# Performance work log

Hardware: AMD Instinct MI355X
Metric: run time of the kernel (lower is better)

## Reference

```python
import jax, jax.numpy as jnp
import numpy as np

# Static configuration (matches init_kwargs)
NW, WH, WW, SH, SW = 1024, 8, 8, 2, 2
EMBED, NH = 192, 6
HD = EMBED // NH            # 32
NP = WH * WW                # 64 patches per window
S2 = SH * SW                # 4 shuffle groups
L = NP * S2                 # 256 tokens per window
NWM = 64                    # number of mask windows
SCALE = HD ** (-0.5) / SH   # head_dim**-0.5 / shuffle
EPS = 1e-5


def _rel_pos_index():
    # Swin-style relative position index for an (8,8) window.
    coords = np.stack(np.meshgrid(np.arange(WH), np.arange(WW), indexing='ij')).reshape(2, -1)
    rel = (coords[:, :, None] - coords[:, None, :]).transpose(1, 2, 0)  # (64,64,2)
    rel[..., 0] += WH - 1
    rel[..., 0] *= 2 * WW - 1
    rel[..., 1] += WW - 1
    return jnp.asarray(rel.sum(-1).reshape(-1))  # (4096,) values in [0, 225)

REL_IDX = _rel_pos_index()


def _group(x):
    # 'nw (wh sh ww sw) ch -> nw (wh ww) (sh sw) ch'
    return x.reshape(NW, WH, SH, WW, SW, EMBED).transpose(0, 1, 3, 2, 4, 5).reshape(NW, NP, S2, EMBED)


def _ungroup(x):
    # 'nw (wh ww) (sh sw) ch -> nw (wh sh ww sw) ch'
    return x.reshape(NW, WH, WW, SH, SW, EMBED).transpose(0, 1, 3, 2, 4, 5).reshape(NW, L, EMBED)


def _ln(x, w, b):
    # LayerNorm over the last two dims [shuffle**2, embed_dim]
    mu = x.mean(axis=(-2, -1), keepdims=True)
    var = x.var(axis=(-2, -1), keepdims=True)
    return (x - mu) * jax.lax.rsqrt(var + EPS) * w + b


def _heads(x):
    # 'nw np s2 (nh hd) -> nw nh np s2 hd'
    return x.reshape(NW, NP, S2, NH, HD).transpose(0, 3, 1, 2, 4)


def setup_inputs() -> dict:
    key = jax.random.key(0)
    ks = jax.random.split(key, 7)
    inp = {
        'query': jax.random.normal(ks[0], (NW, L, EMBED), jnp.float32),
        'key': jax.random.normal(ks[1], (NW, L, EMBED), jnp.float32),
        'value': jax.random.normal(ks[2], (NW, L, EMBED), jnp.float32),
        'mask': jax.random.normal(ks[3], (NWM, NP, NP), jnp.float32),
        'ln_q_w': jnp.ones((S2, EMBED), jnp.float32),
        'ln_q_b': jnp.zeros((S2, EMBED), jnp.float32),
        'ln_k_w': jnp.ones((S2, EMBED), jnp.float32),
        'ln_k_b': jnp.zeros((S2, EMBED), jnp.float32),
        'ln_v_w': jnp.ones((S2, EMBED), jnp.float32),
        'ln_v_b': jnp.zeros((S2, EMBED), jnp.float32),
        'bias_table': 0.02 * jax.random.normal(ks[4], ((2 * WH - 1) * (2 * WW - 1), NH), jnp.float32),
        'proj_w': 0.02 * jax.random.normal(ks[5], (EMBED, EMBED), jnp.float32),  # nn.Linear weight (out,in)
    }
    return inp


def reference(query, key, value, mask, ln_q_w, ln_q_b, ln_k_w, ln_k_b, ln_v_w, ln_v_b, bias_table, proj_w):
    q = _heads(_ln(_group(query), ln_q_w, ln_q_b)) * SCALE   # (nw,nh,np,s2,hd)
    k = _heads(_ln(_group(key), ln_k_w, ln_k_b))
    v = _heads(_ln(_group(value), ln_v_w, ln_v_b))

    attn = jnp.einsum('whqsc,whksc->whqk', q, k)              # (nw,nh,np,np)

    bias = bias_table[REL_IDX].reshape(NP, NP, NH).transpose(2, 0, 1)  # (nh,np,np)
    attn = attn + bias[None]

    b = NW // NWM
    attn = (attn.reshape(b, NWM, NH, NP, NP) + mask[None, :, None]).reshape(NW, NH, NP, NP)

    attn = jax.nn.softmax(attn, axis=-1)

    out = jnp.einsum('whqk,whksc->whqsc', attn, v)            # (nw,nh,np,s2,hd)
    out = out.transpose(0, 2, 3, 1, 4).reshape(NW, NP, S2, EMBED)
    out = _ungroup(out)                                       # (nw, L, embed)
    return out @ proj_w.T
```

## Files before the change

### kernel.cpp

```cpp
#include <hip/hip_runtime.h>

#define NWIN 1024
#define LTOK 256
#define EMB  192
#define NPAT 64
#define NHEAD 6
#define HDIM 32
#define SCALE 0.08838834764831845f
#define LN_EPS 1e-5f

typedef float f32x4 __attribute__((ext_vector_type(4)));
typedef short s16x8 __attribute__((ext_vector_type(8)));

#define OFF_KH  0
#define OFF_VT  16384
#define OFF_PB  32768
#define OFF_OB  40960
#define OFF_ST  57856
#define OFF_BH  59392
#define OFF_HB  60416
#define SMEM_BYTES 61440
#define OBSTRIDE 264

__device__ __forceinline__ unsigned short f2bf(float f) {
    unsigned u = __float_as_uint(f);
    u += 0x7fffu + ((u >> 16) & 1u);
    return (unsigned short)(u >> 16);
}

__device__ __forceinline__ int tok_of(int p, int s) {
    return ((p >> 3) << 5) + ((s >> 1) << 4) + ((p & 7) << 1) + (s & 1);
}

__device__ __forceinline__ f32x4 mfma16(s16x8 a, s16x8 b, f32x4 c) {
    return __builtin_amdgcn_mfma_f32_16x16x32_bf16(a, b, c, 0, 0, 0);
}

__device__ __forceinline__ s16x8 ln_pack8r(const float* v, float mu, float rs,
                                           const float* __restrict__ wl,
                                           const float* __restrict__ bl,
                                           float scale) {
    f32x4 w0 = *(const f32x4*)wl;
    f32x4 w1 = *(const f32x4*)(wl + 4);
    f32x4 c0 = *(const f32x4*)bl;
    f32x4 c1 = *(const f32x4*)(bl + 4);
    s16x8 r;
    r[0] = (short)f2bf(((v[0]-mu)*rs*w0[0] + c0[0])*scale);
    r[1] = (short)f2bf(((v[1]-mu)*rs*w0[1] + c0[1])*scale);
    r[2] = (short)f2bf(((v[2]-mu)*rs*w0[2] + c0[2])*scale);
    r[3] = (short)f2bf(((v[3]-mu)*rs*w0[3] + c0[3])*scale);
    r[4] = (short)f2bf(((v[4]-mu)*rs*w1[0] + c1[0])*scale);
    r[5] = (short)f2bf(((v[5]-mu)*rs*w1[1] + c1[1])*scale);
    r[6] = (short)f2bf(((v[6]-mu)*rs*w1[2] + c1[2])*scale);
    r[7] = (short)f2bf(((v[7]-mu)*rs*w1[3] + c1[3])*scale);
    return r;
}

__device__ __forceinline__ void ln_f8r(const float* v, float mu, float rs,
                                       const float* __restrict__ wl,
                                       const float* __restrict__ bl,
                                       float* o) {
    f32x4 w0 = *(const f32x4*)wl;
    f32x4 w1 = *(const f32x4*)(wl + 4);
    f32x4 c0 = *(const f32x4*)bl;
    f32x4 c1 = *(const f32x4*)(bl + 4);
    o[0] = (v[0]-mu)*rs*w0[0] + c0[0];
    o[1] = (v[1]-mu)*rs*w0[1] + c0[1];
    o[2] = (v[2]-mu)*rs*w0[2] + c0[2];
    o[3] = (v[3]-mu)*rs*w0[3] + c0[3];
    o[4] = (v[4]-mu)*rs*w1[0] + c1[0];
    o[5] = (v[5]-mu)*rs*w1[1] + c1[1];
    o[6] = (v[6]-mu)*rs*w1[2] + c1[2];
    o[7] = (v[7]-mu)*rs*w1[3] + c1[3];
}

__device__ __forceinline__ void load_T8(const float* __restrict__ g, size_t wbase,
                                        int tid, int hh, float pre[2][8]) {
    int p = tid & 63;
    #pragma unroll
    for (int i = 0; i < 2; ++i) {
        int scb = (tid >> 6) * 2 + i;
        int s = scb >> 2, cbx = scb & 3;
        int t = tok_of(p, s);
        const float* gp = g + wbase + t*EMB + hh*HDIM + cbx*8;
        *(f32x4*)&pre[i][0] = *(const f32x4*)gp;
        *(f32x4*)&pre[i][4] = *(const f32x4*)(gp + 4);
    }
}

__device__ __forceinline__ void stage_K(char* smem, int tid, int hh,
                                        const float kpre[2][8], const float* stats,
                                        const float* __restrict__ lnkw,
                                        const float* __restrict__ lnkb) {
    const float* muk = stats + 128; const float* rsk = stats + 192;
    int p = tid & 63;
    #pragma unroll
    for (int i = 0; i < 2; ++i) {
        int scb = (tid >> 6) * 2 + i;
        int s = scb >> 2, cbx = scb & 3;
        int chb = hh*HDIM + cbx*8;
        s16x8 kk = ln_pack8r(kpre[i], muk[p], rsk[p],
                             lnkw + s*EMB + chb, lnkb + s*EMB + chb, 1.0f);
        *(s16x8*)(smem + OFF_KH + p*256 + ((scb*16) ^ ((p & 7) << 4))) = kk;
    }
}

__device__ __forceinline__ void stage_V(char* smem, int tid, int hh,
                                        const float vpre[2][8], const float* stats,
                                        const float* __restrict__ lnvw,
                                        const float* __restrict__ lnvb) {
    const float* muv = stats + 256; const float* rsv = stats + 320;
    int p = tid & 63;
    #pragma unroll
    for (int i = 0; i < 2; ++i) {
        int scb = (tid >> 6) * 2 + i;
        int s = scb >> 2, cbx = scb & 3;
        int chb = hh*HDIM + cbx*8;
        float vn[8];
        ln_f8r(vpre[i], muv[p], rsv[p], lnvw + s*EMB + chb, lnvb + s*EMB + chb, vn);
        #pragma unroll
        for (int j = 0; j < 8; ++j) {
            int sc = scb*8 + j;
            *(unsigned short*)(smem + OFF_VT + sc*128 + ((p*2) ^ ((sc & 7) << 4)))
                = f2bf(vn[j]);
        }
    }
}


__global__ __launch_bounds__(512, 2) void dwa_attn_kernel(
    const float* __restrict__ q_g, const float* __restrict__ k_g,
    const float* __restrict__ v_g, const float* __restrict__ mask_g,
    const float* __restrict__ lnqw, const float* __restrict__ lnqb,
    const float* __restrict__ lnkw, const float* __restrict__ lnkb,
    const float* __restrict__ lnvw, const float* __restrict__ lnvb,
    const float* __restrict__ btab, float* __restrict__ out_g)
{
    __shared__ __align__(16) char smem[SMEM_BYTES];

    const int tid  = threadIdx.x;
    const int lane = tid & 63;
    const int wv   = tid >> 6;
    const int win  = blockIdx.x;
    const size_t wbase = (size_t)win * LTOK * EMB;
    char* preb = (char*)out_g + (size_t)win * 196608 + 98304;

    float* stats = (float*)(smem + OFF_ST);
    float* muq = stats;       float* rsq = stats + 64;
    float* biash = (float*)(smem + OFF_BH);
    float2* HB = (float2*)(smem + OFF_HB);

    const int mstrip = wv >> 1, nhalf = wv & 1;
    const int l15 = lane & 15, l4 = lane >> 4;
    const int pr = mstrip*16 + l15;
    const int cb = l4;

    const float* mask_w = mask_g + (size_t)(win & 63) * NPAT * NPAT;
    const int kc0 = nhalf*32 + l15, kc1 = kc0 + 16;
    float mm0[4], mm1[4];
    int idx0[4], idx1[4];
    {
        int kh0 = kc0 >> 3, kw0 = kc0 & 7, kh1 = kc1 >> 3, kw1 = kc1 & 7;
        #pragma unroll
        for (int r = 0; r < 4; ++r) {
            int qr = mstrip*16 + l4*4 + r;
            mm0[r] = mask_w[qr*64 + kc0];
            mm1[r] = mask_w[qr*64 + kc1];
            idx0[r] = ((qr>>3) - kh0 + 7)*15 + ((qr&7) - kw0 + 7);
            idx1[r] = ((qr>>3) - kh1 + 7)*15 + ((qr&7) - kw1 + 7);
        }
    }

    {
        float* part = (float*)(smem + OFF_OB);
        const int t = tid >> 1, half = tid & 1;
        const f32x4* qp = (const f32x4*)(q_g + wbase + t*EMB + half*96);
        const f32x4* kp = (const f32x4*)(k_g + wbase + t*EMB + half*96);
        const f32x4* vp = (const f32x4*)(v_g + wbase + t*EMB + half*96);
        float s1q=0.f,s2q=0.f,s1k=0.f,s2k=0.f,s1v=0.f,s2v=0.f;
        #pragma unroll 4
        for (int i = 0; i < 24; ++i) {
            f32x4 a = qp[i];
            s1q += a[0]+a[1]+a[2]+a[3];
            s2q += a[0]*a[0]+a[1]*a[1]+a[2]*a[2]+a[3]*a[3];
            f32x4 b = kp[i];
            s1k += b[0]+b[1]+b[2]+b[3];
            s2k += b[0]*b[0]+b[1]*b[1]+b[2]*b[2]+b[3]*b[3];
            f32x4 c = vp[i];
            s1v += c[0]+c[1]+c[2]+c[3];
            s2v += c[0]*c[0]+c[1]*c[1]+c[2]*c[2]+c[3]*c[3];
        }
        float* pp = part + (t*2 + half)*6;
        pp[0]=s1q; pp[1]=s2q; pp[2]=s1k; pp[3]=s2k; pp[4]=s1v; pp[5]=s2v;
        __syncthreads();
        if (tid < NPAT) {
            float S[6] = {0.f,0.f,0.f,0.f,0.f,0.f};
            #pragma unroll
            for (int s = 0; s < 4; ++s) {
                int tt = tok_of(tid, s);
                const float* pr_ = part + tt*12;
                #pragma unroll
                for (int x = 0; x < 6; ++x) S[x] += pr_[x] + pr_[6 + x];
            }
            #pragma unroll
            for (int x = 0; x < 3; ++x) {
                float mu  = S[2*x] * (1.f/768.f);
                float var = S[2*x+1] * (1.f/768.f) - mu*mu;
                stats[x*128 + tid]      = mu;
                stats[x*128 + 64 + tid] = rsqrtf(var + LN_EPS);
            }
        }
        __syncthreads();
    }

    float kpre[2][8], vpre[2][8];
    float breg;
    load_T8(k_g, wbase, tid, 0, kpre);
    load_T8(v_g, wbase, tid, 0, vpre);
    breg = (tid < 225) ? btab[tid * NHEAD] : 0.f;
    stage_K(smem, tid, 0, kpre, stats, lnkw, lnkb);
    stage_V(smem, tid, 0, vpre, stats, lnvw, lnvb);
    if (tid < 225) biash[tid] = breg;
    __syncthreads();

    for (int h = 0; h < NHEAD; ++h) {
        const bool pf = (h < NHEAD-1);
        if (pf) {
            load_T8(k_g, wbase, tid, h+1, kpre);
            load_T8(v_g, wbase, tid, h+1, vpre);
            breg = (tid < 225) ? btab[tid*NHEAD + h + 1] : 0.f;
        }

        float e0[4], e1[4], mrow[4];
        {
            float mu = muq[pr], rs = rsq[pr];
            const float* qbase = q_g + wbase + h*HDIM + cb*8;
            f32x4 acc0 = {0.f,0.f,0.f,0.f};
            f32x4 acc1 = {0.f,0.f,0.f,0.f};
            #pragma unroll
            for (int ks = 0; ks < 4; ++ks) {
                int t = tok_of(pr, ks);
                float qv[8];
                *(f32x4*)&qv[0] = *(const f32x4*)(qbase + t*EMB);
                *(f32x4*)&qv[4] = *(const f32x4*)(qbase + t*EMB + 4);
                int chb = h*HDIM + cb*8;
                s16x8 af = ln_pack8r(qv, mu, rs,
                                     lnqw + ks*EMB + chb, lnqb + ks*EMB + chb, SCALE);
                {
                    int row = nhalf*32 + l15;
                    s16x8 bf = *(const s16x8*)(smem + OFF_KH + row*256 +
                                  ((ks*64 + cb*16) ^ ((row & 7) << 4)));
                    acc0 = mfma16(af, bf, acc0);
                }
                {
                    int row = nhalf*32 + 16 + l15;
                    s16x8 bf = *(const s16x8*)(smem + OFF_KH + row*256 +
                                  ((ks*64 + cb*16) ^ ((row & 7) << 4)));
                    acc1 = mfma16(af, bf, acc1);
                }
            }
            float srow[4];
            #pragma unroll
            for (int r = 0; r < 4; ++r) {
                float L0 = acc0[r] + mm0[r] + biash[idx0[r]];
                float L1 = acc1[r] + mm1[r] + biash[idx1[r]];
                float m = fmaxf(L0, L1);
                m = fmaxf(m, __shfl_xor(m, 1));
                m = fmaxf(m, __shfl_xor(m, 2));
                m = fmaxf(m, __shfl_xor(m, 4));
                m = fmaxf(m, __shfl_xor(m, 8));
                float a = __expf(L0 - m), b = __expf(L1 - m);
                float s = a + b;
                s += __shfl_xor(s, 1);
                s += __shfl_xor(s, 2);
                s += __shfl_xor(s, 4);
                s += __shfl_xor(s, 8);
                e0[r] = a; e1[r] = b; mrow[r] = m; srow[r] = s;
            }
            if (l15 == 0) {
                #pragma unroll
                for (int r = 0; r < 4; ++r) {
                    float2 v; v.x = mrow[r]; v.y = srow[r];
                    HB[(mstrip*16 + l4*4 + r)*2 + nhalf] = v;
                }
            }
        }
        __syncthreads();

        if (pf) {
            stage_K(smem, tid, h+1, kpre, stats, lnkw, lnkb);
            if (tid < 225) biash[tid] = breg;
        }
        #pragma unroll
        for (int r = 0; r < 4; ++r) {
            int qr = mstrip*16 + l4*4 + r;
            float2 ha = HB[qr*2 + 0], hb = HB[qr*2 + 1];
            float M = fmaxf(ha.x, hb.x);
            float tot = ha.y*__expf(ha.x - M) + hb.y*__expf(hb.x - M);
            float f = __expf(mrow[r] - M) / tot;
            unsigned short p0 = f2bf(e0[r]*f);
            unsigned short p1 = f2bf(e1[r]*f);
            *(unsigned short*)(smem + OFF_PB + qr*128 + ((kc0*2) ^ ((qr & 7) << 4))) = p0;
            *(unsigned short*)(smem + OFF_PB + qr*128 + ((kc1*2) ^ ((qr & 7) << 4))) = p1;
        }
        __syncthreads();

        {
            s16x8 ap0 = *(const s16x8*)(smem + OFF_PB + pr*128 +
                          ((cb*16) ^ ((pr & 7) << 4)));
            s16x8 ap1 = *(const s16x8*)(smem + OFF_PB + pr*128 +
                          ((64 + cb*16) ^ ((pr & 7) << 4)));
            __builtin_amdgcn_s_setprio(1);
            #pragma unroll
            for (int i = 0; i < 4; ++i) {
                int nt = nhalf*4 + i;
                int brow = nt*16 + l15;
                f32x4 acc = {0.f,0.f,0.f,0.f};
                s16x8 bf0 = *(const s16x8*)(smem + OFF_VT + brow*128 +
                              ((cb*16) ^ ((brow & 7) << 4)));
                s16x8 bf1 = *(const s16x8*)(smem + OFF_VT + brow*128 +
                              ((64 + cb*16) ^ ((brow & 7) << 4)));
                acc = mfma16(ap0, bf0, acc);
                acc = mfma16(ap1, bf1, acc);
                int sc = nt*16 + l15;
                #pragma unroll
                for (int r = 0; r < 4; ++r) {
                    int qp = mstrip*16 + l4*4 + r;
                    *(unsigned short*)(smem + OFF_OB + qp*OBSTRIDE + sc*2) = f2bf(acc[r]);
                }
            }
            __builtin_amdgcn_s_setprio(0);
        }
        __syncthreads();

        #pragma unroll
        for (int i = 0; i < 2; ++i) {
            int c = i*512 + tid;
            int qp = c >> 4, ch = c & 15;
            s16x8 v = *(const s16x8*)(smem + OFF_OB + qp*OBSTRIDE + ch*16);
            *(s16x8*)(preb + h*16384 + qp*256 + ch*16) = v;
        }
        if (pf) stage_V(smem, tid, h+1, vpre, stats, lnvw, lnvb);
    }
}

__global__ __launch_bounds__(256, 2) void dwa_proj_kernel(
    const float* __restrict__ pw, float* __restrict__ out_g)
{
    __shared__ __align__(16) char smem[73728];

    const int tid  = threadIdx.x;
    const int lane = tid & 63;
    const int wv   = tid >> 6;
    const int w    = blockIdx.x;
    const char* preb = (const char*)out_g + (size_t)w * 196608 + 98304;
    const int cb = lane >> 4;

    s16x8 af[4][6];
    #pragma unroll
    for (int si = 0; si < 4; ++si) {
        int t = (wv*4 + si)*16 + (lane & 15);
        int qp = ((t >> 5) << 3) | ((t >> 1) & 7);
        int s  = (((t >> 4) & 1) << 1) | (t & 1);
        #pragma unroll
        for (int ks = 0; ks < 6; ++ks)
            af[si][ks] = *(const s16x8*)(preb + ks*16384 + qp*256 + s*64 + cb*16);
    }

    #pragma unroll 2
    for (int i = 0; i < 18; ++i) {
        int c = i*256 + tid;
        int orow = c / 24, cb8 = c % 24;
        const float* wp = pw + (size_t)orow*EMB + cb8*8;
        f32x4 a = *(const f32x4*)wp;
        f32x4 b = *(const f32x4*)(wp + 4);
        s16x8 w8;
        w8[0] = (short)f2bf(a[0]); w8[1] = (short)f2bf(a[1]);
        w8[2] = (short)f2bf(a[2]); w8[3] = (short)f2bf(a[3]);
        w8[4] = (short)f2bf(b[0]); w8[5] = (short)f2bf(b[1]);
        w8[6] = (short)f2bf(b[2]); w8[7] = (short)f2bf(b[3]);
        *(s16x8*)(smem + orow*384 + ((cb8*16) ^ ((orow & 7) << 4))) = w8;
    }
    __syncthreads();

    #pragma unroll
    for (int si = 0; si < 4; ++si) {
        int strip = wv*4 + si;
        #pragma unroll
        for (int nt = 0; nt < 12; ++nt) {
            int orow = nt*16 + (lane & 15);
            f32x4 acc = {0.f,0.f,0.f,0.f};
            #pragma unroll
            for (int ks = 0; ks < 6; ++ks) {
                s16x8 bf = *(const s16x8*)(smem + orow*384 +
                              ((ks*64 + cb*16) ^ ((orow & 7) << 4)));
                acc = mfma16(af[si][ks], bf, acc);
            }
            #pragma unroll
            for (int r = 0; r < 4; ++r) {
                int trow = strip*16 + (lane >> 4)*4 + r;
                out_g[(size_t)w*49152 + trow*EMB + nt*16 + (lane & 15)] = acc[r];
            }
        }
    }
}

extern "C" void kernel_launch(void* const* d_in, const int* in_sizes, int n_in,
                              void* d_out, int out_size, void* d_ws, size_t ws_size,
                              hipStream_t stream) {
    (void)in_sizes; (void)n_in; (void)out_size; (void)d_ws; (void)ws_size;
    dwa_attn_kernel<<<dim3(NWIN), dim3(512), 0, stream>>>(
        (const float*)d_in[0],  (const float*)d_in[1],  (const float*)d_in[2],
        (const float*)d_in[3],  (const float*)d_in[4],  (const float*)d_in[5],
        (const float*)d_in[6],  (const float*)d_in[7],  (const float*)d_in[8],
        (const float*)d_in[9],  (const float*)d_in[10],
        (float*)d_out);
    dwa_proj_kernel<<<dim3(NWIN), dim3(256), 0, stream>>>(
        (const float*)d_in[11], (float*)d_out);
}
```

Measured before the change: 452.0 us.

## Restructure attention loop: transposed QK, direct K loads, double-buffered V

Computes S^T by swapping operand roles, so K is LayerNormed directly from global memory into MFMA A-fragments and the K staging buffer in shared memory goes away. The bias table is gathered per head straight from global memory instead of through shared memory. Softmax is restructured so rows reduce across lane groups, with normalization deferred to the PV epilogue, which removes one barrier per head. V is double-buffered so the next head's V staging overlaps the current PV step, and launch bounds are raised to 4 blocks per CU. In exchange, K and bias loads from global/L2 are repeated by each wave.

```diff
diff --git a/kernel.cpp b/kernel.cpp
--- a/kernel.cpp
+++ b/kernel.cpp
@@ -12,15 +12,14 @@
 typedef float f32x4 __attribute__((ext_vector_type(4)));
 typedef short s16x8 __attribute__((ext_vector_type(8)));
 
-#define OFF_KH  0
-#define OFF_VT  16384
+#define OFF_VT0 0
+#define OFF_VT1 16384
 #define OFF_PB  32768
 #define OFF_OB  40960
-#define OFF_ST  57856
-#define OFF_BH  59392
-#define OFF_HB  60416
-#define SMEM_BYTES 61440
-#define OBSTRIDE 264
+#define OFF_ST  58368
+#define OFF_HB  59904
+#define SMEM_BYTES 60928
+#define OBSTRIDE 272
 
 __device__ __forceinline__ unsigned short f2bf(float f) {
     unsigned u = __float_as_uint(f);
@@ -74,61 +73,42 @@
     o[7] = (v[7]-mu)*rs*w1[3] + c1[3];
 }
 
-__device__ __forceinline__ void load_T8(const float* __restrict__ g, size_t wbase,
-                                        int tid, int hh, float pre[2][8]) {
+__device__ __forceinline__ void vload(float vld[2][8], const float* __restrict__ v_g,
+                                      size_t wbase, int tid, int hh) {
     int p = tid & 63;
     #pragma unroll
     for (int i = 0; i < 2; ++i) {
         int scb = (tid >> 6) * 2 + i;
         int s = scb >> 2, cbx = scb & 3;
-        int t = tok_of(p, s);
-        const float* gp = g + wbase + t*EMB + hh*HDIM + cbx*8;
-        *(f32x4*)&pre[i][0] = *(const f32x4*)gp;
-        *(f32x4*)&pre[i][4] = *(const f32x4*)(gp + 4);
-    }
-}
-
-__device__ __forceinline__ void stage_K(char* smem, int tid, int hh,
-                                        const float kpre[2][8], const float* stats,
-                                        const float* __restrict__ lnkw,
-                                        const float* __restrict__ lnkb) {
-    const float* muk = stats + 128; const float* rsk = stats + 192;
+        const float* vp = v_g + wbase + tok_of(p, s)*EMB + hh*HDIM + cbx*8;
+        *(f32x4*)&vld[i][0] = *(const f32x4*)vp;
+        *(f32x4*)&vld[i][4] = *(const f32x4*)(vp + 4);
+    }
+}
+
+__device__ __forceinline__ void vstage(char* vt, const float vld[2][8], int tid, int hh,
+                                       const float* stats,
+                                       const float* __restrict__ lnvw,
+                                       const float* __restrict__ lnvb) {
     int p = tid & 63;
-    #pragma unroll
-    for (int i = 0; i < 2; ++i) {
-        int scb = (tid >> 6) * 2 + i;
-        int s = scb >> 2, cbx = scb & 3;
-        int chb = hh*HDIM + cbx*8;
-        s16x8 kk = ln_pack8r(kpre[i], muk[p], rsk[p],
-                             lnkw + s*EMB + chb, lnkb + s*EMB + chb, 1.0f);
-        *(s16x8*)(smem + OFF_KH + p*256 + ((scb*16) ^ ((p & 7) << 4))) = kk;
-    }
-}
-
-__device__ __forceinline__ void stage_V(char* smem, int tid, int hh,
-                                        const float vpre[2][8], const float* stats,
-                                        const float* __restrict__ lnvw,
-                                        const float* __restrict__ lnvb) {
-    const float* muv = stats + 256; const float* rsv = stats + 320;
-    int p = tid & 63;
+    float muv = stats[256 + p], rsv = stats[320 + p];
     #pragma unroll
     for (int i = 0; i < 2; ++i) {
         int scb = (tid >> 6) * 2 + i;
         int s = scb >> 2, cbx = scb & 3;
         int chb = hh*HDIM + cbx*8;
         float vn[8];
-        ln_f8r(vpre[i], muv[p], rsv[p], lnvw + s*EMB + chb, lnvb + s*EMB + chb, vn);
+        ln_f8r(vld[i], muv, rsv, lnvw + s*EMB + chb, lnvb + s*EMB + chb, vn);
         #pragma unroll
         for (int j = 0; j < 8; ++j) {
             int sc = scb*8 + j;
-            *(unsigned short*)(smem + OFF_VT + sc*128 + ((p*2) ^ ((sc & 7) << 4)))
-                = f2bf(vn[j]);
-        }
-    }
-}
-
-
-__global__ __launch_bounds__(512, 2) void dwa_attn_kernel(
+            *(unsigned short*)(vt + sc*128 + ((p*2) ^ ((sc & 7) << 4))) = f2bf(vn[j]);
+        }
+    }
+}
+
+
+__global__ __launch_bounds__(512, 4) void dwa_attn_kernel(
     const float* __restrict__ q_g, const float* __restrict__ k_g,
     const float* __restrict__ v_g, const float* __restrict__ mask_g,
     const float* __restrict__ lnqw, const float* __restrict__ lnqb,
@@ -146,37 +126,33 @@
     char* preb = (char*)out_g + (size_t)win * 196608 + 98304;
 
     float* stats = (float*)(smem + OFF_ST);
-    float* muq = stats;       float* rsq = stats + 64;
-    float* biash = (float*)(smem + OFF_BH);
-    float2* HB = (float2*)(smem + OFF_HB);
-
-    const int mstrip = wv >> 1, nhalf = wv & 1;
     const int l15 = lane & 15, l4 = lane >> 4;
-    const int pr = mstrip*16 + l15;
-    const int cb = l4;
+    const int qt = wv >> 1, half = wv & 1;
+    const int qA  = qt*16 + l15;
+    const int kA0 = (half*2 + 0)*16 + l15;
+    const int kA1 = kA0 + 16;
 
     const float* mask_w = mask_g + (size_t)(win & 63) * NPAT * NPAT;
-    const int kc0 = nhalf*32 + l15, kc1 = kc0 + 16;
-    float mm0[4], mm1[4];
-    int idx0[4], idx1[4];
+    f32x4 mk0 = *(const f32x4*)(mask_w + qA*64 + (half*2+0)*16 + l4*4);
+    f32x4 mk1 = *(const f32x4*)(mask_w + qA*64 + (half*2+1)*16 + l4*4);
+    int bidx[8];
     {
-        int kh0 = kc0 >> 3, kw0 = kc0 & 7, kh1 = kc1 >> 3, kw1 = kc1 & 7;
-        #pragma unroll
-        for (int r = 0; r < 4; ++r) {
-            int qr = mstrip*16 + l4*4 + r;
-            mm0[r] = mask_w[qr*64 + kc0];
-            mm1[r] = mask_w[qr*64 + kc1];
-            idx0[r] = ((qr>>3) - kh0 + 7)*15 + ((qr&7) - kw0 + 7);
-            idx1[r] = ((qr>>3) - kh1 + 7)*15 + ((qr&7) - kw1 + 7);
-        }
+        int qh = qA >> 3, qw = qA & 7;
+        #pragma unroll
+        for (int kt = 0; kt < 2; ++kt)
+            #pragma unroll
+            for (int r = 0; r < 4; ++r) {
+                int kc = (half*2 + kt)*16 + l4*4 + r;
+                bidx[kt*4+r] = ((qh - (kc>>3) + 7)*15 + (qw - (kc&7) + 7)) * NHEAD;
+            }
     }
 
     {
         float* part = (float*)(smem + OFF_OB);
-        const int t = tid >> 1, half = tid & 1;
-        const f32x4* qp = (const f32x4*)(q_g + wbase + t*EMB + half*96);
-        const f32x4* kp = (const f32x4*)(k_g + wbase + t*EMB + half*96);
-        const f32x4* vp = (const f32x4*)(v_g + wbase + t*EMB + half*96);
+        const int t = tid >> 1, hlf = tid & 1;
+        const f32x4* qp = (const f32x4*)(q_g + wbase + t*EMB + hlf*96);
+        const f32x4* kp = (const f32x4*)(k_g + wbase + t*EMB + hlf*96);
+        const f32x4* vp = (const f32x4*)(v_g + wbase + t*EMB + hlf*96);
         float s1q=0.f,s2q=0.f,s1k=0.f,s2k=0.f,s1v=0.f,s2v=0.f;
         #pragma unroll 4
         for (int i = 0; i < 24; ++i) {
@@ -190,7 +166,7 @@
             s1v += c[0]+c[1]+c[2]+c[3];
             s2v += c[0]*c[0]+c[1]*c[1]+c[2]*c[2]+c[3]*c[3];
         }
-        float* pp = part + (t*2 + half)*6;
+        float* pp = part + (t*2 + hlf)*6;
         pp[0]=s1q; pp[1]=s2q; pp[2]=s1k; pp[3]=s2k; pp[4]=s1v; pp[5]=s2v;
         __syncthreads();
         if (tid < NPAT) {
@@ -213,134 +189,127 @@
         __syncthreads();
     }
 
-    float kpre[2][8], vpre[2][8];
-    float breg;
-    load_T8(k_g, wbase, tid, 0, kpre);
-    load_T8(v_g, wbase, tid, 0, vpre);
-    breg = (tid < 225) ? btab[tid * NHEAD] : 0.f;
-    stage_K(smem, tid, 0, kpre, stats, lnkw, lnkb);
-    stage_V(smem, tid, 0, vpre, stats, lnvw, lnvb);
-    if (tid < 225) biash[tid] = breg;
-    __syncthreads();
+    {
+        float vld[2][8];
+        vload(vld, v_g, wbase, tid, 0);
+        vstage(smem + OFF_VT0, vld, tid, 0, stats, lnvw, lnvb);
+    }
+
+    const float muqv = stats[qA],       rsqv = stats[64 + qA];
+    const float muk0 = stats[128 + kA0], rsk0 = stats[192 + kA0];
+    const float muk1 = stats[128 + kA1], rsk1 = stats[192 + kA1];
 
     for (int h = 0; h < NHEAD; ++h) {
-        const bool pf = (h < NHEAD-1);
-        if (pf) {
-            load_T8(k_g, wbase, tid, h+1, kpre);
-            load_T8(v_g, wbase, tid, h+1, vpre);
-            breg = (tid < 225) ? btab[tid*NHEAD + h + 1] : 0.f;
-        }
-
-        float e0[4], e1[4], mrow[4];
+        float bload[8];
+        #pragma unroll
+        for (int i = 0; i < 8; ++i) bload[i] = btab[bidx[i] + h];
+
+        f32x4 acc0 = {0.f,0.f,0.f,0.f};
+        f32x4 acc1 = {0.f,0.f,0.f,0.f};
         {
-            float mu = muq[pr], rs = rsq[pr];
-            const float* qbase = q_g + wbase + h*HDIM + cb*8;
-            f32x4 acc0 = {0.f,0.f,0.f,0.f};
-            f32x4 acc1 = {0.f,0.f,0.f,0.f};
+            const int ch = h*HDIM + l4*8;
             #pragma unroll
             for (int ks = 0; ks < 4; ++ks) {
-                int t = tok_of(pr, ks);
-                float qv[8];
-                *(f32x4*)&qv[0] = *(const f32x4*)(qbase + t*EMB);
-                *(f32x4*)&qv[4] = *(const f32x4*)(qbase + t*EMB + 4);
-                int chb = h*HDIM + cb*8;
-                s16x8 af = ln_pack8r(qv, mu, rs,
-                                     lnqw + ks*EMB + chb, lnqb + ks*EMB + chb, SCALE);
-                {
-                    int row = nhalf*32 + l15;
-                    s16x8 bf = *(const s16x8*)(smem + OFF_KH + row*256 +
-                                  ((ks*64 + cb*16) ^ ((row & 7) << 4)));
-                    acc0 = mfma16(af, bf, acc0);
-                }
-                {
-                    int row = nhalf*32 + 16 + l15;
-                    s16x8 bf = *(const s16x8*)(smem + OFF_KH + row*256 +
-                                  ((ks*64 + cb*16) ^ ((row & 7) << 4)));
-                    acc1 = mfma16(af, bf, acc1);
-                }
-            }
-            float srow[4];
+                const float* qp_ = q_g + wbase + tok_of(qA,  ks)*EMB + ch;
+                const float* kp0 = k_g + wbase + tok_of(kA0, ks)*EMB + ch;
+                const float* kp1 = k_g + wbase + tok_of(kA1, ks)*EMB + ch;
+                float qv[8], kv0[8], kv1[8];
+                *(f32x4*)&qv[0]  = *(const f32x4*)qp_;
+                *(f32x4*)&qv[4]  = *(const f32x4*)(qp_ + 4);
+                *(f32x4*)&kv0[0] = *(const f32x4*)kp0;
+                *(f32x4*)&kv0[4] = *(const f32x4*)(kp0 + 4);
+                *(f32x4*)&kv1[0] = *(const f32x4*)kp1;
+                *(f32x4*)&kv1[4] = *(const f32x4*)(kp1 + 4);
+                const float* lwq = lnqw + ks*EMB + ch;
+                const float* lbq = lnqb + ks*EMB + ch;
+                const float* lwk = lnkw + ks*EMB + ch;
+                const float* lbk = lnkb + ks*EMB + ch;
+                s16x8 bf = ln_pack8r(qv,  muqv, rsqv, lwq, lbq, SCALE);
+                s16x8 a0 = ln_pack8r(kv0, muk0, rsk0, lwk, lbk, 1.0f);
+                s16x8 a1 = ln_pack8r(kv1, muk1, rsk1, lwk, lbk, 1.0f);
+                acc0 = mfma16(a0, bf, acc0);
+                acc1 = mfma16(a1, bf, acc1);
+            }
+        }
+        {
+            float P[8];
             #pragma unroll
             for (int r = 0; r < 4; ++r) {
-                float L0 = acc0[r] + mm0[r] + biash[idx0[r]];
-                float L1 = acc1[r] + mm1[r] + biash[idx1[r]];
-                float m = fmaxf(L0, L1);
-                m = fmaxf(m, __shfl_xor(m, 1));
-                m = fmaxf(m, __shfl_xor(m, 2));
-                m = fmaxf(m, __shfl_xor(m, 4));
-                m = fmaxf(m, __shfl_xor(m, 8));
-                float a = __expf(L0 - m), b = __expf(L1 - m);
-                float s = a + b;
-                s += __shfl_xor(s, 1);
-                s += __shfl_xor(s, 2);
-                s += __shfl_xor(s, 4);
-                s += __shfl_xor(s, 8);
-                e0[r] = a; e1[r] = b; mrow[r] = m; srow[r] = s;
-            }
-            if (l15 == 0) {
-                #pragma unroll
-                for (int r = 0; r < 4; ++r) {
-                    float2 v; v.x = mrow[r]; v.y = srow[r];
-                    HB[(mstrip*16 + l4*4 + r)*2 + nhalf] = v;
-                }
+                P[r]   = acc0[r] + mk0[r] + bload[r];
+                P[4+r] = acc1[r] + mk1[r] + bload[4+r];
+            }
+            float m = fmaxf(fmaxf(fmaxf(P[0],P[1]), fmaxf(P[2],P[3])),
+                            fmaxf(fmaxf(P[4],P[5]), fmaxf(P[6],P[7])));
+            m = fmaxf(m, __shfl_xor(m, 16));
+            m = fmaxf(m, __shfl_xor(m, 32));
+            float s = 0.f;
+            #pragma unroll
+            for (int i = 0; i < 8; ++i) { P[i] = __expf(P[i] - m); s += P[i]; }
+            s += __shfl_xor(s, 16);
+            s += __shfl_xor(s, 32);
+            if (l4 == 0) {
+                float2 v; v.x = m; v.y = s;
+                *(float2*)(smem + OFF_HB + qA*16 + half*8) = v;
+            }
+            #pragma unroll
+            for (int kt = 0; kt < 2; ++kt) {
+                uint2 pk;
+                pk.x = (unsigned)f2bf(P[kt*4+0]) | ((unsigned)f2bf(P[kt*4+1]) << 16);
+                pk.y = (unsigned)f2bf(P[kt*4+2]) | ((unsigned)f2bf(P[kt*4+3]) << 16);
+                *(uint2*)(smem + OFF_PB + qA*128 +
+                    (((half*2 + kt)*32 + l4*8) ^ ((qA & 7) << 4))) = pk;
             }
         }
         __syncthreads();
 
-        if (pf) {
-            stage_K(smem, tid, h+1, kpre, stats, lnkw, lnkb);
-            if (tid < 225) biash[tid] = breg;
-        }
-        #pragma unroll
-        for (int r = 0; r < 4; ++r) {
-            int qr = mstrip*16 + l4*4 + r;
-            float2 ha = HB[qr*2 + 0], hb = HB[qr*2 + 1];
-            float M = fmaxf(ha.x, hb.x);
-            float tot = ha.y*__expf(ha.x - M) + hb.y*__expf(hb.x - M);
-            float f = __expf(mrow[r] - M) / tot;
-            unsigned short p0 = f2bf(e0[r]*f);
-            unsigned short p1 = f2bf(e1[r]*f);
-            *(unsigned short*)(smem + OFF_PB + qr*128 + ((kc0*2) ^ ((qr & 7) << 4))) = p0;
-            *(unsigned short*)(smem + OFF_PB + qr*128 + ((kc1*2) ^ ((qr & 7) << 4))) = p1;
-        }
-        __syncthreads();
-
+        float vld[2][8];
+        if (h < NHEAD-1) vload(vld, v_g, wbase, tid, h+1);
         {
-            s16x8 ap0 = *(const s16x8*)(smem + OFF_PB + pr*128 +
-                          ((cb*16) ^ ((pr & 7) << 4)));
-            s16x8 ap1 = *(const s16x8*)(smem + OFF_PB + pr*128 +
-                          ((64 + cb*16) ^ ((pr & 7) << 4)));
+            f32x4 hb = *(const f32x4*)(smem + OFF_HB + qA*16);
+            float M  = fmaxf(hb[0], hb[2]);
+            float w0 = __expf(hb[0] - M), w1 = __expf(hb[2] - M);
+            float Sv = 1.f / (hb[1]*w0 + hb[3]*w1);
+            float f0 = w0*Sv, f1 = w1*Sv;
+            s16x8 pb0 = *(const s16x8*)(smem + OFF_PB + qA*128 +
+                          ((l4*16) ^ ((qA & 7) << 4)));
+            s16x8 pb1 = *(const s16x8*)(smem + OFF_PB + qA*128 +
+                          ((64 + l4*16) ^ ((qA & 7) << 4)));
+            const char* vt = smem + ((h & 1) ? OFF_VT1 : OFF_VT0);
             __builtin_amdgcn_s_setprio(1);
             #pragma unroll
             for (int i = 0; i < 4; ++i) {
-                int nt = nhalf*4 + i;
-                int brow = nt*16 + l15;
-                f32x4 acc = {0.f,0.f,0.f,0.f};
-                s16x8 bf0 = *(const s16x8*)(smem + OFF_VT + brow*128 +
-                              ((cb*16) ^ ((brow & 7) << 4)));
-                s16x8 bf1 = *(const s16x8*)(smem + OFF_VT + brow*128 +
-                              ((64 + cb*16) ^ ((brow & 7) << 4)));
-                acc = mfma16(ap0, bf0, acc);
-                acc = mfma16(ap1, bf1, acc);
-                int sc = nt*16 + l15;
-                #pragma unroll
-                for (int r = 0; r < 4; ++r) {
-                    int qp = mstrip*16 + l4*4 + r;
-                    *(unsigned short*)(smem + OFF_OB + qp*OBSTRIDE + sc*2) = f2bf(acc[r]);
-                }
+                int sct = half*4 + i;
+                int scr = sct*16 + l15;
+                s16x8 a0 = *(const s16x8*)(vt + scr*128 +
+                              ((l4*16) ^ ((scr & 7) << 4)));
+                s16x8 a1 = *(const s16x8*)(vt + scr*128 +
+                              ((64 + l4*16) ^ ((scr & 7) << 4)));
+                f32x4 z = {0.f,0.f,0.f,0.f};
+                f32x4 c0 = mfma16(a0, pb0, z);
+                f32x4 c1 = mfma16(a1, pb1, z);
+                float o0 = f0*c0[0] + f1*c1[0];
+                float o1 = f0*c0[1] + f1*c1[1];
+                float o2 = f0*c0[2] + f1*c1[2];
+                float o3 = f0*c0[3] + f1*c1[3];
+                uint2 pk;
+                pk.x = (unsigned)f2bf(o0) | ((unsigned)f2bf(o1) << 16);
+                pk.y = (unsigned)f2bf(o2) | ((unsigned)f2bf(o3) << 16);
+                *(uint2*)(smem + OFF_OB + qA*OBSTRIDE + sct*32 + l4*8) = pk;
             }
             __builtin_amdgcn_s_setprio(0);
         }
+        if (h < NHEAD-1)
+            vstage(smem + ((h & 1) ? OFF_VT0 : OFF_VT1), vld, tid, h+1,
+                   stats, lnvw, lnvb);
         __syncthreads();
 
         #pragma unroll
         for (int i = 0; i < 2; ++i) {
             int c = i*512 + tid;
-            int qp = c >> 4, ch = c & 15;
-            s16x8 v = *(const s16x8*)(smem + OFF_OB + qp*OBSTRIDE + ch*16);
-            *(s16x8*)(preb + h*16384 + qp*256 + ch*16) = v;
-        }
-        if (pf) stage_V(smem, tid, h+1, vpre, stats, lnvw, lnvb);
+            int qp = c >> 4, ch2 = c & 15;
+            s16x8 v = *(const s16x8*)(smem + OFF_OB + qp*OBSTRIDE + ch2*16);
+            *(s16x8*)(preb + h*16384 + qp*256 + ch2*16) = v;
+        }
     }
 }
 
```

New measurement: 655.9 us. 45.1% more time.
